# Kernel optimization log

Hardware: AMD Instinct MI355X
Metric: run time of the kernel (lower is better)

The kernel has to match this reference:

```python
import jax, jax.numpy as jnp
import numpy as np

B, FEAT, SPD_H, CTRL_H, N_CMD = 32768, 512, 128, 256, 4


def _p(key, shape, fan_in):
    # torch nn.Linear default init: U(-1/sqrt(fan_in), 1/sqrt(fan_in))
    lim = 1.0 / np.sqrt(fan_in)
    return jax.random.uniform(key, shape, jnp.float32, -lim, lim)


def setup_inputs() -> dict:
    key = jax.random.key(0)
    ks = iter(jax.random.split(key, 32))
    inp = {
        "feat": jax.random.normal(next(ks), (B, FEAT), jnp.float32),
        "speed": jax.random.uniform(next(ks), (B,), jnp.float32),
        "command": jax.random.randint(next(ks), (B,), 0, N_CMD, jnp.int32),
        "ms_w1": _p(next(ks), (1, SPD_H), 1), "ms_b1": _p(next(ks), (SPD_H,), 1),
        "ms_w2": _p(next(ks), (SPD_H, SPD_H), SPD_H), "ms_b2": _p(next(ks), (SPD_H,), SPD_H),
        "ms_w3": _p(next(ks), (SPD_H, SPD_H), SPD_H), "ms_b3": _p(next(ks), (SPD_H,), SPD_H),
        # speed_pred_module: 512 -> 256 -> 256 -> 1
        "sp_w1": _p(next(ks), (FEAT, CTRL_H), FEAT), "sp_b1": _p(next(ks), (CTRL_H,), FEAT),
        "sp_w2": _p(next(ks), (CTRL_H, CTRL_H), CTRL_H), "sp_b2": _p(next(ks), (CTRL_H,), CTRL_H),
        "sp_w3": _p(next(ks), (CTRL_H, 1), CTRL_H), "sp_b3": _p(next(ks), (1,), CTRL_H),
        # join_module: Linear(640, 512)
        "join_w": _p(next(ks), (FEAT + SPD_H, FEAT), FEAT + SPD_H),
        "join_b": _p(next(ks), (FEAT,), FEAT + SPD_H),
        # 4 control heads: 512 -> 256 -> 256 -> 3 (stacked on expert axis e)
        "ctrl_w1": _p(next(ks), (N_CMD, FEAT, CTRL_H), FEAT), "ctrl_b1": _p(next(ks), (N_CMD, CTRL_H), FEAT),
        "ctrl_w2": _p(next(ks), (N_CMD, CTRL_H, CTRL_H), CTRL_H), "ctrl_b2": _p(next(ks), (N_CMD, CTRL_H), CTRL_H),
        "ctrl_w3": _p(next(ks), (N_CMD, CTRL_H, 3), CTRL_H), "ctrl_b3": _p(next(ks), (N_CMD, 3), CTRL_H),
    }
    return inp


def _mlp(x, w1, b1, w2, b2, w3, b3):
    # FullyConnectedNet: Linear, ReLU, Linear, Dropout(p=0 -> noop), ReLU, Linear
    h = jax.nn.relu(x @ w1 + b1)
    h = jax.nn.relu(h @ w2 + b2)
    return h @ w3 + b3


def reference(feat, speed, command,
              ms_w1, ms_b1, ms_w2, ms_b2, ms_w3, ms_b3,
              sp_w1, sp_b1, sp_w2, sp_b2, sp_w3, sp_b3,
              join_w, join_b,
              ctrl_w1, ctrl_b1, ctrl_w2, ctrl_b2, ctrl_w3, ctrl_b3):
    v = _mlp(speed[:, None], ms_w1, ms_b1, ms_w2, ms_b2, ms_w3, ms_b3)      # [B,128]
    joined = jnp.concatenate([feat, v], axis=1) @ join_w + join_b           # [B,512]
    v_p = _mlp(feat, sp_w1, sp_b1, sp_w2, sp_b2, sp_w3, sp_b3)              # [B,1]
    # command-indexed dispatch: compute all 4 heads densely, then select per sample
    h1 = jax.nn.relu(jnp.einsum('bd,edh->beh', joined, ctrl_w1) + ctrl_b1)  # [B,4,256]
    h2 = jax.nn.relu(jnp.einsum('beh,ehk->bek', h1, ctrl_w2) + ctrl_b2)     # [B,4,256]
    act_all = jnp.einsum('bek,eko->beo', h2, ctrl_w3) + ctrl_b3             # [B,4,3]
    action = jnp.take_along_axis(act_all, command[:, None, None].astype(jnp.int32), axis=1)[:, 0]  # [B,3]
    throttle = jax.nn.sigmoid(action[:, 0])
    steering = jnp.tanh(action[:, 1])
    brake = jax.nn.sigmoid(action[:, 2])
    return v_p, throttle, brake, steering
```

## Files before the change

### kernel.cpp

```cpp
#include <hip/hip_runtime.h>
#include <hip/hip_bf16.h>
#include <stdint.h>
#include <math.h>

#define BB 32768
#define FEAT 512
#define SPD_H 128
#define CTRL_H 256
#define NCMD 4

typedef __attribute__((ext_vector_type(8))) short bf16x8;
typedef __attribute__((ext_vector_type(4))) float f32x4;

__device__ __forceinline__ unsigned short f2bf(float f) {
  union { float f; uint32_t u; } v; v.f = f;
  uint32_t u = v.u;
  return (unsigned short)((u + 0x7fffu + ((u >> 16) & 1u)) >> 16);
}

__device__ __forceinline__ void async16(const unsigned short* g, unsigned short* l) {
  __builtin_amdgcn_global_load_lds(
      (const __attribute__((address_space(1))) unsigned int*)g,
      (__attribute__((address_space(3))) unsigned int*)l, 16, 0, 0);
}

__device__ __forceinline__ void gemm128(
    const unsigned short* __restrict__ A, int lda,
    const int* __restrict__ perm, int m_start, int m_cnt,
    const unsigned short* __restrict__ W, const float* __restrict__ bi,
    unsigned short* __restrict__ C, int ldc, int relu, int K, int mt, int nt) {
  __shared__ unsigned short As[128 * 32];
  __shared__ unsigned short Bs[128 * 32];
  __shared__ float fscr[32][132];

  const int m0 = mt * 128;
  if (m0 >= m_cnt) return;
  const int n0 = nt * 128;
  const int t = threadIdx.x;
  const int w = t >> 6, lane = t & 63;
  const int wm = w & 1, wn = w >> 1;

  f32x4 acc[4][4];
#pragma unroll
  for (int i = 0; i < 4; ++i)
#pragma unroll
    for (int j = 0; j < 4; ++j)
#pragma unroll
      for (int r = 0; r < 4; ++r) acc[i][j][r] = 0.f;

  const int fr = lane & 15;
  const int fk = (lane >> 4) * 8;

  const unsigned short* agp[2]; const unsigned short* bgp[2];
  unsigned short* al[2]; unsigned short* bl[2];
#pragma unroll
  for (int it = 0; it < 2; ++it) {
    int row = w * 32 + it * 16 + (lane >> 2);
    int seg8 = (lane & 3) * 8;
    int rl = m0 + row;
    if (rl >= m_cnt) rl = m_cnt - 1;
    int grow = perm ? perm[m_start + rl] : (m_start + rl);
    agp[it] = A + (size_t)grow * lda + seg8;
    bgp[it] = W + (size_t)(n0 + row) * K + seg8;
    al[it] = As + (w * 32 + it * 16) * 32;
    bl[it] = Bs + (w * 32 + it * 16) * 32;
  }

  for (int k0 = 0; k0 < K; k0 += 32) {
#pragma unroll
    for (int it = 0; it < 2; ++it) {
      async16(agp[it] + k0, al[it]);
      async16(bgp[it] + k0, bl[it]);
    }
    __syncthreads();
    bf16x8 af[4], bfv[4];
#pragma unroll
    for (int i = 0; i < 4; ++i)
      af[i] = *(const bf16x8*)(As + (wm * 64 + i * 16 + fr) * 32 + fk);
#pragma unroll
    for (int j = 0; j < 4; ++j)
      bfv[j] = *(const bf16x8*)(Bs + (wn * 64 + j * 16 + fr) * 32 + fk);
#pragma unroll
    for (int i = 0; i < 4; ++i)
#pragma unroll
      for (int j = 0; j < 4; ++j)
        acc[i][j] = __builtin_amdgcn_mfma_f32_16x16x32_bf16(af[i], bfv[j], acc[i][j], 0, 0, 0);
    __syncthreads();
  }

  const int rquad = (lane >> 4) * 4;
  const int cidx = lane & 15;

  float bv[4];
#pragma unroll
  for (int j = 0; j < 4; ++j) bv[j] = bi ? bi[n0 + wn * 64 + j * 16 + cidx] : 0.f;

#pragma unroll
  for (int c = 0; c < 4; ++c) {
    if (wm == (c >> 1)) {
#pragma unroll
      for (int j = 0; j < 4; ++j) {
#pragma unroll
        for (int ii = 0; ii < 2; ++ii) {
          int i = 2 * (c & 1) + ii;
          int lr = ii * 16 + rquad;
#pragma unroll
          for (int r = 0; r < 4; ++r) {
            float v = acc[i][j][r] + bv[j];
            if (relu) v = fmaxf(v, 0.f);
            fscr[lr + r][wn * 64 + j * 16 + cidx] = v;
          }
        }
      }
    }
    __syncthreads();
#pragma unroll
    for (int q = 0; q < 2; ++q) {
      int sg = t + 256 * q;
      int lr = sg >> 4, cs = (sg & 15) * 8;
      int grow = m0 + c * 32 + lr;
      if (grow < m_cnt) {
        union { bf16x8 v; unsigned short u[8]; } pk;
#pragma unroll
        for (int x = 0; x < 8; ++x) pk.u[x] = f2bf(fscr[lr][cs + x]);
        *(bf16x8*)(C + (size_t)(m_start + grow) * ldc + (n0 + cs)) = pk.v;
      }
    }
    __syncthreads();
  }
}

struct WSeg { const float* src; unsigned short* dst; int K; int N; int ldd; };
struct PrepArgs {
  WSeg s[12];
  int start[13];
  const float* join_w; unsigned short* wjbf;
  const float* feat; unsigned short* ajoin;
  const int* cmd; int* wavecnt;
  const float* join_b; const float* ctrl_w1; const float* ctrl_b1; float* b_f;
};
__global__ void k_prep(PrepArgs a) {
  int bx = blockIdx.x, t = threadIdx.x;
  if (bx < 16384) {
    int idx = bx * 256 + t;
    int i = idx >> 7;
    int j4 = (idx & 127) << 2;
    float4 f = *(const float4*)(a.feat + (size_t)i * FEAT + j4);
    ushort4 o;
    o.x = f2bf(f.x); o.y = f2bf(f.y); o.z = f2bf(f.z); o.w = f2bf(f.w);
    *(ushort4*)(a.ajoin + (size_t)i * 640 + j4) = o;
    return;
  }
  int rel = bx - 16384;
  if (rel < 320) {
    int idx = rel * 256 + t;
    float4 f = *(const float4*)(a.join_w + (size_t)idx * 4);
    ushort4 o;
    o.x = f2bf(f.x); o.y = f2bf(f.y); o.z = f2bf(f.z); o.w = f2bf(f.w);
    *(ushort4*)(a.wjbf + (size_t)idx * 4) = o;
    return;
  }
  rel -= 320;
  if (rel < a.start[12]) {
    int si = 0;
    while (rel >= a.start[si + 1]) ++si;
    WSeg sg = a.s[si];
    int tile = rel - a.start[si];
    int tkx = sg.K >> 5;
    int tn = tile / tkx;
    int tk = tile - tn * tkx;
    int k0 = tk * 32, n0 = tn * 32;
    __shared__ float tb[32][33];
    int tx = t & 31, ty = t >> 5;
#pragma unroll
    for (int j = 0; j < 4; ++j)
      tb[ty + j * 8][tx] = sg.src[(size_t)(k0 + ty + j * 8) * sg.N + n0 + tx];
    __syncthreads();
#pragma unroll
    for (int j = 0; j < 4; ++j)
      sg.dst[(size_t)(n0 + ty + j * 8) * sg.ldd + k0 + tx] = f2bf(tb[tx][ty + j * 8]);
    return;
  }
  rel -= a.start[12];
  if (rel < 128) {
    int i = rel * 256 + t;
    int c = a.cmd[i];
    int wid = i >> 6;
    int lane = t & 63;
#pragma unroll
    for (int cv = 0; cv < NCMD; ++cv) {
      unsigned long long m = __ballot(c == cv);
      if (lane == 0) a.wavecnt[cv * 512 + wid] = __popcll(m);
    }
    return;
  }
  int e = rel - 128;
  float s = a.ctrl_b1[e * 256 + t];
  const float* w = a.ctrl_w1 + (size_t)e * 512 * 256 + t;
  for (int m = 0; m < 512; ++m) s = fmaf(a.join_b[m], w[(size_t)m * 256], s);
  a.b_f[e * 256 + t] = s;
}

__launch_bounds__(256)
__global__ void k_ms(const float* __restrict__ speed,
                     const float* __restrict__ w1, const float* __restrict__ b1,
                     const unsigned short* __restrict__ w2t, const float* __restrict__ b2,
                     const unsigned short* __restrict__ w3t, const float* __restrict__ b3,
                     unsigned short* __restrict__ ajoin) {
  __shared__ unsigned short hw[128][136];
  __shared__ unsigned short Bs[128 * 32];
  const int m0 = blockIdx.x * 128;
  const int t = threadIdx.x;
  const int w = t >> 6, lane = t & 63;
  const int wm = w & 1, wn = w >> 1;
  const int fr = lane & 15, fk = (lane >> 4) * 8;
  const int rquad = (lane >> 4) * 4, cidx = lane & 15;

  {
    int r = t >> 1, half = t & 1;
    float s = speed[m0 + r];
#pragma unroll
    for (int c0 = 0; c0 < 64; c0 += 4) {
      int c = half * 64 + c0;
      float4 wv = *(const float4*)(w1 + c);
      float4 bv = *(const float4*)(b1 + c);
      hw[r][c + 0] = f2bf(fmaxf(fmaf(s, wv.x, bv.x), 0.f));
      hw[r][c + 1] = f2bf(fmaxf(fmaf(s, wv.y, bv.y), 0.f));
      hw[r][c + 2] = f2bf(fmaxf(fmaf(s, wv.z, bv.z), 0.f));
      hw[r][c + 3] = f2bf(fmaxf(fmaf(s, wv.w, bv.w), 0.f));
    }
  }
  __syncthreads();

  for (int layer = 0; layer < 2; ++layer) {
    const unsigned short* Wt = layer ? w3t : w2t;
    const float* bb = layer ? b3 : b2;
    f32x4 acc[4][4];
#pragma unroll
    for (int i = 0; i < 4; ++i)
#pragma unroll
      for (int j = 0; j < 4; ++j)
#pragma unroll
        for (int r = 0; r < 4; ++r) acc[i][j][r] = 0.f;

    for (int k0 = 0; k0 < 128; k0 += 32) {
#pragma unroll
      for (int it = 0; it < 2; ++it) {
        int row = w * 32 + it * 16 + (lane >> 2);
        async16(Wt + (size_t)row * 128 + k0 + (lane & 3) * 8,
                Bs + (w * 32 + it * 16) * 32);
      }
      __syncthreads();
      bf16x8 af[4], bfv[4];
#pragma unroll
      for (int i = 0; i < 4; ++i)
        af[i] = *(const bf16x8*)(&hw[wm * 64 + i * 16 + fr][k0 + fk]);
#pragma unroll
      for (int j = 0; j < 4; ++j)
        bfv[j] = *(const bf16x8*)(Bs + (wn * 64 + j * 16 + fr) * 32 + fk);
#pragma unroll
      for (int i = 0; i < 4; ++i)
#pragma unroll
        for (int j = 0; j < 4; ++j)
          acc[i][j] = __builtin_amdgcn_mfma_f32_16x16x32_bf16(af[i], bfv[j], acc[i][j], 0, 0, 0);
      __syncthreads();
    }
#pragma unroll
    for (int j = 0; j < 4; ++j) {
      int col = wn * 64 + j * 16 + cidx;
      float bv = bb[col];
#pragma unroll
      for (int i = 0; i < 4; ++i) {
        int row = wm * 64 + i * 16 + rquad;
#pragma unroll
        for (int r = 0; r < 4; ++r) {
          float v = acc[i][j][r] + bv;
          if (layer == 0) v = fmaxf(v, 0.f);
          hw[row + r][col] = f2bf(v);
        }
      }
    }
    __syncthreads();
  }
  {
    int r = t >> 1, half = t & 1;
#pragma unroll
    for (int c8 = 0; c8 < 8; ++c8)
      *(bf16x8*)(ajoin + (size_t)(m0 + r) * 640 + 512 + half * 64 + c8 * 8) =
          *(const bf16x8*)(&hw[r][half * 64 + c8 * 8]);
  }
}

struct MidArgs {
  const int* cmd; const int* wavecnt; int* perm; int* offs;
  const unsigned short* c_w1t; const unsigned short* wjbf; unsigned short* wf_t;
};
__launch_bounds__(256)
__global__ void k_mid(MidArgs a) {
  int b = blockIdx.x, t = threadIdx.x;
  if (b >= 128) {
    int idx = b - 128;
    int mt = idx & 7, nt = idx >> 3;
    gemm128(a.c_w1t, 512, nullptr, 0, 1024, a.wjbf, nullptr, a.wf_t, 640, 0, 512, mt, nt);
    return;
  }
  __shared__ int pf[NCMD][4];
  __shared__ int tot[NCMD];
  int c = t >> 6, lane = t & 63;
  int v[8]; int s = 0;
#pragma unroll
  for (int q = 0; q < 8; ++q) { v[q] = a.wavecnt[c * 512 + lane * 8 + q]; s += v[q]; }
  int p = s;
#pragma unroll
  for (int m = 1; m < 64; m <<= 1) { int o = __shfl_up(p, m, 64); if (lane >= m) p += o; }
  int excl = p - s;
  if (lane == 63) tot[c] = p;
  if (lane == ((4 * b) >> 3)) {
    int base_off = (4 * b) & 7;
    int run = excl;
#pragma unroll
    for (int q = 0; q < 8; ++q) {
      if (q >= base_off && q < base_off + 4) pf[c][q - base_off] = run;
      run += v[q];
    }
  }
  __syncthreads();
  int soffs[NCMD + 1];
  soffs[0] = 0;
#pragma unroll
  for (int e = 0; e < NCMD; ++e) soffs[e + 1] = soffs[e] + tot[e];
  if (b == 0 && t == 0)
    for (int e = 0; e <= NCMD; ++e) a.offs[e] = soffs[e];
  int i = b * 256 + t;
  int mc = a.cmd[i];
  int lwid = t >> 6;
  int rank = 0, base = 0;
#pragma unroll
  for (int cv = 0; cv < NCMD; ++cv) {
    unsigned long long m = __ballot(mc == cv);
    if (mc == cv) {
      rank = __popcll(m & ((1ull << lane) - 1ull));
      base = soffs[cv] + pf[cv][lwid];
    }
  }
  a.perm[base + rank] = i;
}

struct MainArgs {
  const unsigned short* ajoin;
  const unsigned short* wf_t; const float* b_f;
  const unsigned short* sp_w1t; const float* sp_b1;
  unsigned short* ch1; unsigned short* sph1;
  const int* perm; const int* seg;
};
__launch_bounds__(256)
__global__ void k_main(MainArgs a) {
  const int z = blockIdx.z;
  const int gid = blockIdx.x;
  const int mt = gid & 255, nt = gid >> 8;
  if (z == 4) {
    gemm128(a.ajoin, 640, nullptr, 0, BB, a.sp_w1t, a.sp_b1, a.sph1, 256, 1, 512, mt, nt);
  } else {
    int ms = a.seg[z], mc = a.seg[z + 1] - ms;
    gemm128(a.ajoin, 640, a.perm, ms, mc, a.wf_t + (size_t)z * 256 * 640,
            a.b_f + z * 256, a.ch1, 256, 1, 640, mt, nt);
  }
}

struct VArgs {
  const unsigned short* A_s; const unsigned short* A_c;
  const unsigned short* W_s; const unsigned short* W_c;
  const float* b_s; const float* b_c;
  const float* w3_s; const float* b3_s;
  const float* w3_c; const float* b3_c;
  const int* perm; const int* seg;
  float* out;
};
__launch_bounds__(256)
__global__ void k_vgemm(VArgs a) {
  __shared__ unsigned short As[64 * 32];
  __shared__ unsigned short Bs[256 * 32];
  const int z = blockIdx.z;
  const unsigned short* A; const unsigned short* W; const float* bi;
  int m_start, m_cnt;
  if (z == 4) { A = a.A_s; W = a.W_s; bi = a.b_s; m_start = 0; m_cnt = BB; }
  else {
    A = a.A_c; W = a.W_c + (size_t)z * 65536; bi = a.b_c + z * 256;
    m_start = a.seg[z]; m_cnt = a.seg[z + 1] - m_start;
  }
  const int m0 = blockIdx.x * 64;
  if (m0 >= m_cnt) return;
  const int t = threadIdx.x, w = t >> 6, lane = t & 63;
  const int fr = lane & 15, fk = (lane >> 4) * 8;

  f32x4 acc[16];
#pragma unroll
  for (int j = 0; j < 16; ++j)
#pragma unroll
    for (int r = 0; r < 4; ++r) acc[j][r] = 0.f;

  int arow = m0 + w * 16 + (lane >> 2);
  if (arow >= m_cnt) arow = m_cnt - 1;
  const unsigned short* ap = A + (size_t)(m_start + arow) * 256 + (lane & 3) * 8;
  unsigned short* al = As + (w * 16) * 32;
  const unsigned short* bp[4]; unsigned short* bl[4];
#pragma unroll
  for (int it = 0; it < 4; ++it) {
    int brow = w * 64 + it * 16 + (lane >> 2);
    bp[it] = W + (size_t)brow * 256 + (lane & 3) * 8;
    bl[it] = Bs + (w * 64 + it * 16) * 32;
  }

  for (int k0 = 0; k0 < 256; k0 += 32) {
    async16(ap + k0, al);
#pragma unroll
    for (int it = 0; it < 4; ++it) async16(bp[it] + k0, bl[it]);
    __syncthreads();
    bf16x8 af = *(const bf16x8*)(As + (w * 16 + fr) * 32 + fk);
#pragma unroll
    for (int j = 0; j < 16; ++j) {
      bf16x8 bfv = *(const bf16x8*)(Bs + (j * 16 + fr) * 32 + fk);
      acc[j] = __builtin_amdgcn_mfma_f32_16x16x32_bf16(af, bfv, acc[j], 0, 0, 0);
    }
    __syncthreads();
  }

  const int rquad = (lane >> 4) * 4;
  float bcol[16];
#pragma unroll
  for (int j = 0; j < 16; ++j) bcol[j] = bi[j * 16 + fr];

  if (z == 4) {
    float aw[16];
#pragma unroll
    for (int j = 0; j < 16; ++j) aw[j] = a.w3_s[j * 16 + fr];
#pragma unroll
    for (int r = 0; r < 4; ++r) {
      float s = 0.f;
#pragma unroll
      for (int j = 0; j < 16; ++j)
        s = fmaf(fmaxf(acc[j][r] + bcol[j], 0.f), aw[j], s);
      s += __shfl_xor(s, 1, 64);
      s += __shfl_xor(s, 2, 64);
      s += __shfl_xor(s, 4, 64);
      s += __shfl_xor(s, 8, 64);
      int row = m0 + w * 16 + rquad + r;
      if (fr == 0 && row < m_cnt) a.out[row] = s + a.b3_s[0];
    }
  } else {
    float aw0[16], aw1[16], aw2[16];
#pragma unroll
    for (int j = 0; j < 16; ++j) {
      const float* wp = a.w3_c + (size_t)z * 768 + (j * 16 + fr) * 3;
      aw0[j] = wp[0]; aw1[j] = wp[1]; aw2[j] = wp[2];
    }
#pragma unroll
    for (int r = 0; r < 4; ++r) {
      float s0 = 0.f, s1 = 0.f, s2 = 0.f;
#pragma unroll
      for (int j = 0; j < 16; ++j) {
        float v = fmaxf(acc[j][r] + bcol[j], 0.f);
        s0 = fmaf(v, aw0[j], s0);
        s1 = fmaf(v, aw1[j], s1);
        s2 = fmaf(v, aw2[j], s2);
      }
#pragma unroll
      for (int m = 1; m <= 8; m <<= 1) {
        s0 += __shfl_xor(s0, m, 64);
        s1 += __shfl_xor(s1, m, 64);
        s2 += __shfl_xor(s2, m, 64);
      }
      int row = m0 + w * 16 + rquad + r;
      if (fr == 0 && row < m_cnt) {
        int orig = a.perm[m_start + row];
        float a0 = s0 + a.b3_c[z * 3 + 0];
        float a1 = s1 + a.b3_c[z * 3 + 1];
        float a2 = s2 + a.b3_c[z * 3 + 2];
        a.out[BB + orig]     = 1.f / (1.f + __expf(-a0));
        a.out[2 * BB + orig] = 1.f / (1.f + __expf(-a2));
        a.out[3 * BB + orig] = tanhf(a1);
      }
    }
  }
}

static inline size_t align256(size_t x) { return (x + 255) & ~(size_t)255; }

extern "C" void kernel_launch(void* const* d_in, const int* in_sizes, int n_in,
                              void* d_out, int out_size, void* d_ws, size_t ws_size,
                              hipStream_t stream) {
  const float* feat   = (const float*)d_in[0];
  const float* speed  = (const float*)d_in[1];
  const int*   command= (const int*)d_in[2];
  const float* ms_w1  = (const float*)d_in[3];
  const float* ms_b1  = (const float*)d_in[4];
  const float* ms_w2  = (const float*)d_in[5];
  const float* ms_b2  = (const float*)d_in[6];
  const float* ms_w3  = (const float*)d_in[7];
  const float* ms_b3  = (const float*)d_in[8];
  const float* sp_w1  = (const float*)d_in[9];
  const float* sp_b1  = (const float*)d_in[10];
  const float* sp_w2  = (const float*)d_in[11];
  const float* sp_b2  = (const float*)d_in[12];
  const float* sp_w3  = (const float*)d_in[13];
  const float* sp_b3  = (const float*)d_in[14];
  const float* join_w = (const float*)d_in[15];
  const float* join_b = (const float*)d_in[16];
  const float* ctrl_w1= (const float*)d_in[17];
  const float* ctrl_b1= (const float*)d_in[18];
  const float* ctrl_w2= (const float*)d_in[19];
  const float* ctrl_b2= (const float*)d_in[20];
  const float* ctrl_w3= (const float*)d_in[21];
  const float* ctrl_b3= (const float*)d_in[22];
  float* out = (float*)d_out;

  char* ws = (char*)d_ws;
  size_t off = 0;
  auto alloc = [&](size_t bytes) -> char* { char* p = ws + off; off = align256(off + bytes); return p; };

  unsigned short* ajoin  = (unsigned short*)alloc((size_t)BB * 640 * 2);
  unsigned short* sph1   = (unsigned short*)alloc((size_t)BB * 256 * 2);
  unsigned short* ch1    = (unsigned short*)alloc((size_t)BB * 256 * 2);
  unsigned short* wtp    = (unsigned short*)alloc(1998848ull * 2);
  int* perm    = (int*)alloc((size_t)BB * 4);
  int* cnt     = (int*)alloc(64);
  int* wavecnt = (int*)alloc(4 * 512 * 4);
  float* b_f   = (float*)alloc(4 * 256 * 4);

  unsigned short* sp_w1t = wtp;
  unsigned short* sp_w2t = wtp + 131072;
  unsigned short* ms_w2t = wtp + 196608;
  unsigned short* ms_w3t = wtp + 212992;
  unsigned short* c_w1t  = wtp + 229376;
  unsigned short* c_w2t  = wtp + 753664;
  unsigned short* wjbf   = wtp + 1015808;
  unsigned short* wf_t   = wtp + 1343488;

  PrepArgs P;
  P.s[0] = { sp_w1, sp_w1t, 512, 256, 512 };
  P.s[1] = { sp_w2, sp_w2t, 256, 256, 256 };
  P.s[2] = { ms_w2, ms_w2t, 128, 128, 128 };
  P.s[3] = { ms_w3, ms_w3t, 128, 128, 128 };
  for (int e = 0; e < 4; ++e) P.s[4 + e] = { ctrl_w1 + (size_t)e * 512 * 256, c_w1t + (size_t)e * 131072, 512, 256, 512 };
  for (int e = 0; e < 4; ++e) P.s[8 + e] = { ctrl_w2 + (size_t)e * 256 * 256, c_w2t + (size_t)e * 65536, 256, 256, 256 };
  P.start[0] = 0;
  for (int i = 0; i < 12; ++i)
    P.start[i + 1] = P.start[i] + (P.s[i].K >> 5) * (P.s[i].N >> 5);
  P.join_w = join_w; P.wjbf = wjbf;
  P.feat = feat; P.ajoin = ajoin;
  P.cmd = command; P.wavecnt = wavecnt;
  P.join_b = join_b; P.ctrl_w1 = ctrl_w1; P.ctrl_b1 = ctrl_b1; P.b_f = b_f;
  int prep_blocks = 16384 + 320 + P.start[12] + 128 + 4;

  k_prep<<<prep_blocks, 256, 0, stream>>>(P);
  k_ms<<<256, 256, 0, stream>>>(speed, ms_w1, ms_b1, ms_w2t, ms_b2, ms_w3t, ms_b3, ajoin);

  MidArgs Mi;
  Mi.cmd = command; Mi.wavecnt = wavecnt; Mi.perm = perm; Mi.offs = cnt + 4;
  Mi.c_w1t = c_w1t; Mi.wjbf = wjbf; Mi.wf_t = wf_t;
  k_mid<<<168, 256, 0, stream>>>(Mi);

  MainArgs Ma;
  Ma.ajoin = ajoin; Ma.wf_t = wf_t; Ma.b_f = b_f;
  Ma.sp_w1t = sp_w1t; Ma.sp_b1 = sp_b1;
  Ma.ch1 = ch1; Ma.sph1 = sph1;
  Ma.perm = perm; Ma.seg = cnt + 4;
  k_main<<<dim3(512, 1, 5), 256, 0, stream>>>(Ma);

  VArgs V;
  V.A_s = sph1; V.A_c = ch1; V.W_s = sp_w2t; V.W_c = c_w2t;
  V.b_s = sp_b2; V.b_c = ctrl_b2;
  V.w3_s = sp_w3; V.b3_s = sp_b3; V.w3_c = ctrl_w3; V.b3_c = ctrl_b3;
  V.perm = perm; V.seg = cnt + 4; V.out = out;
  k_vgemm<<<dim3(512, 1, 5), 256, 0, stream>>>(V);
}
```

Before: 248.2 us.

## Fold speed MLP into k_mid, reuse bf16 LDS epilogue, and permute speed-pred GEMM

Moves the measured-speed MLP blocks into the k_mid launch as extra blocks, removing one kernel launch. The gemm128 epilogue now converts to bf16 before staging in a reused dynamic LDS buffer, which shrinks shared memory and allows more occupancy. The speed-prediction first layer is computed over permuted rows alongside each expert's segment in a 2D grid, and the final scalar output is scattered back through perm. This adds more grid blocks, of which many exit early, and changes the sph1 row ordering to permuted order.

New measurement: 237.6 us. 1.04x faster.

```diff
diff --git a/kernel.cpp b/kernel.cpp
--- a/kernel.cpp
+++ b/kernel.cpp
@@ -29,9 +29,9 @@
     const int* __restrict__ perm, int m_start, int m_cnt,
     const unsigned short* __restrict__ W, const float* __restrict__ bi,
     unsigned short* __restrict__ C, int ldc, int relu, int K, int mt, int nt) {
-  __shared__ unsigned short As[128 * 32];
-  __shared__ unsigned short Bs[128 * 32];
-  __shared__ float fscr[32][132];
+  extern __shared__ __align__(16) unsigned char dynsm[];
+  unsigned short* As = (unsigned short*)dynsm;
+  unsigned short* Bs = As + 128 * 32;
 
   const int m0 = mt * 128;
   if (m0 >= m_cnt) return;
@@ -95,6 +95,7 @@
 #pragma unroll
   for (int j = 0; j < 4; ++j) bv[j] = bi ? bi[n0 + wn * 64 + j * 16 + cidx] : 0.f;
 
+  unsigned short (*bscr)[136] = (unsigned short(*)[136])dynsm;
 #pragma unroll
   for (int c = 0; c < 4; ++c) {
     if (wm == (c >> 1)) {
@@ -108,7 +109,7 @@
           for (int r = 0; r < 4; ++r) {
             float v = acc[i][j][r] + bv[j];
             if (relu) v = fmaxf(v, 0.f);
-            fscr[lr + r][wn * 64 + j * 16 + cidx] = v;
+            bscr[lr + r][wn * 64 + j * 16 + cidx] = f2bf(v);
           }
         }
       }
@@ -119,12 +120,9 @@
       int sg = t + 256 * q;
       int lr = sg >> 4, cs = (sg & 15) * 8;
       int grow = m0 + c * 32 + lr;
-      if (grow < m_cnt) {
-        union { bf16x8 v; unsigned short u[8]; } pk;
-#pragma unroll
-        for (int x = 0; x < 8; ++x) pk.u[x] = f2bf(fscr[lr][cs + x]);
-        *(bf16x8*)(C + (size_t)(m_start + grow) * ldc + (n0 + cs)) = pk.v;
-      }
+      if (grow < m_cnt)
+        *(bf16x8*)(C + (size_t)(m_start + grow) * ldc + (n0 + cs)) =
+            *(const bf16x8*)(&bscr[lr][cs]);
     }
     __syncthreads();
   }
@@ -139,6 +137,7 @@
   const int* cmd; int* wavecnt;
   const float* join_b; const float* ctrl_w1; const float* ctrl_b1; float* b_f;
 };
+__launch_bounds__(256)
 __global__ void k_prep(PrepArgs a) {
   int bx = blockIdx.x, t = threadIdx.x;
   if (bx < 16384) {
@@ -162,6 +161,7 @@
   }
   rel -= 320;
   if (rel < a.start[12]) {
+    __shared__ float tb[32][33];
     int si = 0;
     while (rel >= a.start[si + 1]) ++si;
     WSeg sg = a.s[si];
@@ -170,7 +170,6 @@
     int tn = tile / tkx;
     int tk = tile - tn * tkx;
     int k0 = tk * 32, n0 = tn * 32;
-    __shared__ float tb[32][33];
     int tx = t & 31, ty = t >> 5;
 #pragma unroll
     for (int j = 0; j < 4; ++j)
@@ -201,103 +200,100 @@
   a.b_f[e * 256 + t] = s;
 }
 
-__launch_bounds__(256)
-__global__ void k_ms(const float* __restrict__ speed,
-                     const float* __restrict__ w1, const float* __restrict__ b1,
-                     const unsigned short* __restrict__ w2t, const float* __restrict__ b2,
-                     const unsigned short* __restrict__ w3t, const float* __restrict__ b3,
-                     unsigned short* __restrict__ ajoin) {
-  __shared__ unsigned short hw[128][136];
-  __shared__ unsigned short Bs[128 * 32];
-  const int m0 = blockIdx.x * 128;
-  const int t = threadIdx.x;
-  const int w = t >> 6, lane = t & 63;
-  const int wm = w & 1, wn = w >> 1;
-  const int fr = lane & 15, fk = (lane >> 4) * 8;
-  const int rquad = (lane >> 4) * 4, cidx = lane & 15;
-
-  {
-    int r = t >> 1, half = t & 1;
-    float s = speed[m0 + r];
-#pragma unroll
-    for (int c0 = 0; c0 < 64; c0 += 4) {
-      int c = half * 64 + c0;
-      float4 wv = *(const float4*)(w1 + c);
-      float4 bv = *(const float4*)(b1 + c);
-      hw[r][c + 0] = f2bf(fmaxf(fmaf(s, wv.x, bv.x), 0.f));
-      hw[r][c + 1] = f2bf(fmaxf(fmaf(s, wv.y, bv.y), 0.f));
-      hw[r][c + 2] = f2bf(fmaxf(fmaf(s, wv.z, bv.z), 0.f));
-      hw[r][c + 3] = f2bf(fmaxf(fmaf(s, wv.w, bv.w), 0.f));
-    }
-  }
-  __syncthreads();
-
-  for (int layer = 0; layer < 2; ++layer) {
-    const unsigned short* Wt = layer ? w3t : w2t;
-    const float* bb = layer ? b3 : b2;
-    f32x4 acc[4][4];
-#pragma unroll
-    for (int i = 0; i < 4; ++i)
-#pragma unroll
-      for (int j = 0; j < 4; ++j)
-#pragma unroll
-        for (int r = 0; r < 4; ++r) acc[i][j][r] = 0.f;
-
-    for (int k0 = 0; k0 < 128; k0 += 32) {
-#pragma unroll
-      for (int it = 0; it < 2; ++it) {
-        int row = w * 32 + it * 16 + (lane >> 2);
-        async16(Wt + (size_t)row * 128 + k0 + (lane & 3) * 8,
-                Bs + (w * 32 + it * 16) * 32);
-      }
-      __syncthreads();
-      bf16x8 af[4], bfv[4];
-#pragma unroll
-      for (int i = 0; i < 4; ++i)
-        af[i] = *(const bf16x8*)(&hw[wm * 64 + i * 16 + fr][k0 + fk]);
-#pragma unroll
-      for (int j = 0; j < 4; ++j)
-        bfv[j] = *(const bf16x8*)(Bs + (wn * 64 + j * 16 + fr) * 32 + fk);
-#pragma unroll
-      for (int i = 0; i < 4; ++i)
-#pragma unroll
-        for (int j = 0; j < 4; ++j)
-          acc[i][j] = __builtin_amdgcn_mfma_f32_16x16x32_bf16(af[i], bfv[j], acc[i][j], 0, 0, 0);
-      __syncthreads();
-    }
-#pragma unroll
-    for (int j = 0; j < 4; ++j) {
-      int col = wn * 64 + j * 16 + cidx;
-      float bv = bb[col];
-#pragma unroll
-      for (int i = 0; i < 4; ++i) {
-        int row = wm * 64 + i * 16 + rquad;
-#pragma unroll
-        for (int r = 0; r < 4; ++r) {
-          float v = acc[i][j][r] + bv;
-          if (layer == 0) v = fmaxf(v, 0.f);
-          hw[row + r][col] = f2bf(v);
-        }
-      }
-    }
-    __syncthreads();
-  }
-  {
-    int r = t >> 1, half = t & 1;
-#pragma unroll
-    for (int c8 = 0; c8 < 8; ++c8)
-      *(bf16x8*)(ajoin + (size_t)(m0 + r) * 640 + 512 + half * 64 + c8 * 8) =
-          *(const bf16x8*)(&hw[r][half * 64 + c8 * 8]);
-  }
-}
-
 struct MidArgs {
   const int* cmd; const int* wavecnt; int* perm; int* offs;
   const unsigned short* c_w1t; const unsigned short* wjbf; unsigned short* wf_t;
+  const float* speed;
+  const float* ms_w1; const float* ms_b1;
+  const unsigned short* ms_w2t; const float* ms_b2;
+  const unsigned short* ms_w3t; const float* ms_b3;
+  unsigned short* ajoin;
 };
 __launch_bounds__(256)
 __global__ void k_mid(MidArgs a) {
   int b = blockIdx.x, t = threadIdx.x;
+  if (b >= 168) {
+    extern __shared__ __align__(16) unsigned char dynsm[];
+    unsigned short (*hw)[136] = (unsigned short(*)[136])dynsm;
+    unsigned short* BsM = (unsigned short*)(dynsm + 128 * 136 * 2);
+    const int m0 = (b - 168) * 128;
+    const int w = t >> 6, lane = t & 63;
+    const int wm = w & 1, wn = w >> 1;
+    const int fr = lane & 15, fk = (lane >> 4) * 8;
+    const int rquad = (lane >> 4) * 4, cidx = lane & 15;
+    {
+      int r = t >> 1, half = t & 1;
+      float s = a.speed[m0 + r];
+#pragma unroll
+      for (int c0 = 0; c0 < 64; c0 += 4) {
+        int c = half * 64 + c0;
+        float4 wv = *(const float4*)(a.ms_w1 + c);
+        float4 bv = *(const float4*)(a.ms_b1 + c);
+        hw[r][c + 0] = f2bf(fmaxf(fmaf(s, wv.x, bv.x), 0.f));
+        hw[r][c + 1] = f2bf(fmaxf(fmaf(s, wv.y, bv.y), 0.f));
+        hw[r][c + 2] = f2bf(fmaxf(fmaf(s, wv.z, bv.z), 0.f));
+        hw[r][c + 3] = f2bf(fmaxf(fmaf(s, wv.w, bv.w), 0.f));
+      }
+    }
+    __syncthreads();
+    for (int layer = 0; layer < 2; ++layer) {
+      const unsigned short* Wt = layer ? a.ms_w3t : a.ms_w2t;
+      const float* bb = layer ? a.ms_b3 : a.ms_b2;
+      f32x4 acc[4][4];
+#pragma unroll
+      for (int i = 0; i < 4; ++i)
+#pragma unroll
+        for (int j = 0; j < 4; ++j)
+#pragma unroll
+          for (int r = 0; r < 4; ++r) acc[i][j][r] = 0.f;
+      for (int k0 = 0; k0 < 128; k0 += 32) {
+#pragma unroll
+        for (int it = 0; it < 2; ++it) {
+          int row = w * 32 + it * 16 + (lane >> 2);
+          async16(Wt + (size_t)row * 128 + k0 + (lane & 3) * 8,
+                  BsM + (w * 32 + it * 16) * 32);
+        }
+        __syncthreads();
+        bf16x8 af[4], bfv[4];
+#pragma unroll
+        for (int i = 0; i < 4; ++i)
+          af[i] = *(const bf16x8*)(&hw[wm * 64 + i * 16 + fr][k0 + fk]);
+#pragma unroll
+        for (int j = 0; j < 4; ++j)
+          bfv[j] = *(const bf16x8*)(BsM + (wn * 64 + j * 16 + fr) * 32 + fk);
+#pragma unroll
+        for (int i = 0; i < 4; ++i)
+#pragma unroll
+          for (int j = 0; j < 4; ++j)
+            acc[i][j] = __builtin_amdgcn_mfma_f32_16x16x32_bf16(af[i], bfv[j], acc[i][j], 0, 0, 0);
+        __syncthreads();
+      }
+#pragma unroll
+      for (int j = 0; j < 4; ++j) {
+        int col = wn * 64 + j * 16 + cidx;
+        float bv = bb[col];
+#pragma unroll
+        for (int i = 0; i < 4; ++i) {
+          int row = wm * 64 + i * 16 + rquad;
+#pragma unroll
+          for (int r = 0; r < 4; ++r) {
+            float v = acc[i][j][r] + bv;
+            if (layer == 0) v = fmaxf(v, 0.f);
+            hw[row + r][col] = f2bf(v);
+          }
+        }
+      }
+      __syncthreads();
+    }
+    {
+      int r = t >> 1, half = t & 1;
+#pragma unroll
+      for (int c8 = 0; c8 < 8; ++c8)
+        *(bf16x8*)(a.ajoin + (size_t)(m0 + r) * 640 + 512 + half * 64 + c8 * 8) =
+            *(const bf16x8*)(&hw[r][half * 64 + c8 * 8]);
+    }
+    return;
+  }
   if (b >= 128) {
     int idx = b - 128;
     int mt = idx & 7, nt = idx >> 3;
@@ -350,20 +346,21 @@
   const unsigned short* ajoin;
   const unsigned short* wf_t; const float* b_f;
   const unsigned short* sp_w1t; const float* sp_b1;
-  unsigned short* ch1; unsigned short* sph1;
+  unsigned short* ch1; unsigned short* sph1p;
   const int* perm; const int* seg;
 };
 __launch_bounds__(256)
 __global__ void k_main(MainArgs a) {
-  const int z = blockIdx.z;
+  const int e = blockIdx.z;
   const int gid = blockIdx.x;
   const int mt = gid & 255, nt = gid >> 8;
-  if (z == 4) {
-    gemm128(a.ajoin, 640, nullptr, 0, BB, a.sp_w1t, a.sp_b1, a.sph1, 256, 1, 512, mt, nt);
+  int ms = a.seg[e], mc = a.seg[e + 1] - ms;
+  if (nt < 2) {
+    gemm128(a.ajoin, 640, a.perm, ms, mc, a.wf_t + (size_t)e * 256 * 640,
+            a.b_f + e * 256, a.ch1, 256, 1, 640, mt, nt);
   } else {
-    int ms = a.seg[z], mc = a.seg[z + 1] - ms;
-    gemm128(a.ajoin, 640, a.perm, ms, mc, a.wf_t + (size_t)z * 256 * 640,
-            a.b_f + z * 256, a.ch1, 256, 1, 640, mt, nt);
+    gemm128(a.ajoin, 640, a.perm, ms, mc, a.sp_w1t, a.sp_b1,
+            a.sph1p, 256, 1, 512, mt, nt - 2);
   }
 }
 
@@ -445,7 +442,8 @@
       s += __shfl_xor(s, 4, 64);
       s += __shfl_xor(s, 8, 64);
       int row = m0 + w * 16 + rquad + r;
-      if (fr == 0 && row < m_cnt) a.out[row] = s + a.b3_s[0];
+      if (fr == 0 && row < m_cnt)
+        a.out[a.perm[row]] = s + a.b3_s[0];
     }
   } else {
     float aw0[16], aw1[16], aw2[16];
@@ -519,7 +517,7 @@
   auto alloc = [&](size_t bytes) -> char* { char* p = ws + off; off = align256(off + bytes); return p; };
 
   unsigned short* ajoin  = (unsigned short*)alloc((size_t)BB * 640 * 2);
-  unsigned short* sph1   = (unsigned short*)alloc((size_t)BB * 256 * 2);
+  unsigned short* sph1p  = (unsigned short*)alloc((size_t)BB * 256 * 2);
   unsigned short* ch1    = (unsigned short*)alloc((size_t)BB * 256 * 2);
   unsigned short* wtp    = (unsigned short*)alloc(1998848ull * 2);
   int* perm    = (int*)alloc((size_t)BB * 4);
@@ -553,22 +551,26 @@
   int prep_blocks = 16384 + 320 + P.start[12] + 128 + 4;
 
   k_prep<<<prep_blocks, 256, 0, stream>>>(P);
-  k_ms<<<256, 256, 0, stream>>>(speed, ms_w1, ms_b1, ms_w2t, ms_b2, ms_w3t, ms_b3, ajoin);
 
   MidArgs Mi;
   Mi.cmd = command; Mi.wavecnt = wavecnt; Mi.perm = perm; Mi.offs = cnt + 4;
   Mi.c_w1t = c_w1t; Mi.wjbf = wjbf; Mi.wf_t = wf_t;
-  k_mid<<<168, 256, 0, stream>>>(Mi);
+  Mi.speed = speed;
+  Mi.ms_w1 = ms_w1; Mi.ms_b1 = ms_b1;
+  Mi.ms_w2t = ms_w2t; Mi.ms_b2 = ms_b2;
+  Mi.ms_w3t = ms_w3t; Mi.ms_b3 = ms_b3;
+  Mi.ajoin = ajoin;
+  k_mid<<<168 + 256, 256, 128 * 136 * 2 + 128 * 32 * 2, stream>>>(Mi);
 
   MainArgs Ma;
   Ma.ajoin = ajoin; Ma.wf_t = wf_t; Ma.b_f = b_f;
   Ma.sp_w1t = sp_w1t; Ma.sp_b1 = sp_b1;
-  Ma.ch1 = ch1; Ma.sph1 = sph1;
+  Ma.ch1 = ch1; Ma.sph1p = sph1p;
   Ma.perm = perm; Ma.seg = cnt + 4;
-  k_main<<<dim3(512, 1, 5), 256, 0, stream>>>(Ma);
+  k_main<<<dim3(1024, 1, 4), 256, 128 * 32 * 2 * 2, stream>>>(Ma);
 
   VArgs V;
-  V.A_s = sph1; V.A_c = ch1; V.W_s = sp_w2t; V.W_c = c_w2t;
+  V.A_s = sph1p; V.A_c = ch1; V.W_s = sp_w2t; V.W_c = c_w2t;
   V.b_s = sp_b2; V.b_c = ctrl_b2;
   V.w3_s = sp_w3; V.b3_s = sp_b3; V.w3_c = ctrl_w3; V.b3_c = ctrl_b3;
   V.perm = perm; V.seg = cnt + 4; V.out = out;
```
